# Optimization experiments

Hardware: AMD Instinct MI355X
Metric: run time of the kernel (lower is better)

Reference implementation:

```python
import jax, jax.numpy as jnp
import numpy as np

B, N, M, E, CD, H, DH, MH = 4, 2048, 512, 512, 256, 8, 64, 1024
EPS = 1e-6

def _ln(x):
    m = x.mean(-1, keepdims=True)
    v = ((x - m) ** 2).mean(-1, keepdims=True)
    return (x - m) / jnp.sqrt(v + EPS)

def _heads(t):  # [B, L, H*DH] -> [B, H, L, DH]
    b, l, _ = t.shape
    return t.reshape(b, l, H, DH).transpose(0, 2, 1, 3)

def _attn(q, k, v, scale):
    sim = jnp.einsum('bhid,bhjd->bhij', q, k) * scale
    a = jax.nn.softmax(sim, axis=-1)
    o = jnp.einsum('bhij,bhjd->bhid', a, v)
    b, h, l, d = o.shape
    return o.transpose(0, 2, 1, 3).reshape(b, l, h * d)

def setup_inputs() -> dict:
    key = jax.random.key(0)
    ks = jax.random.split(key, 16)
    s = 0.02
    return {
        'cond': jax.random.normal(ks[0], (B, M, CD), jnp.float32),
        'x_in': jax.random.normal(ks[1], (B, N, E), jnp.float32),
        # nn.MultiheadAttention params (combined in-proj + out-proj)
        'Wqkv': jax.random.normal(ks[2], (3 * E, E), jnp.float32) * s,
        'b_qkv': jnp.zeros((3 * E,), jnp.float32),
        'Wo': jax.random.normal(ks[3], (E, E), jnp.float32) * s,
        'bo': jnp.zeros((E,), jnp.float32),
        # CrossAttention params (q/k/v no bias, out has bias)
        'Wcq': jax.random.normal(ks[4], (H * DH, E), jnp.float32) * s,
        'Wck': jax.random.normal(ks[5], (H * DH, CD), jnp.float32) * s,
        'Wcv': jax.random.normal(ks[6], (H * DH, CD), jnp.float32) * s,
        'Wco': jax.random.normal(ks[7], (E, H * DH), jnp.float32) * s,
        'bco': jnp.zeros((E,), jnp.float32),
        # MLP params (note: ReLU applied after the LAST layer too, per source)
        'W1': jax.random.normal(ks[8], (MH, E), jnp.float32) * s,
        'b1': jnp.zeros((MH,), jnp.float32),
        'W2': jax.random.normal(ks[9], (E, MH), jnp.float32) * s,
        'b2': jnp.zeros((E,), jnp.float32),
    }

def reference(cond, x_in, Wqkv, b_qkv, Wo, bo, Wcq, Wck, Wcv, Wco, bco, W1, b1, W2, b2):
    # --- self-attention (nn.MultiheadAttention math) ---
    xn = _ln(x_in)
    qkv = xn @ Wqkv.T + b_qkv  # [B,N,3E]
    q, k, v = jnp.split(qkv, 3, axis=-1)
    sa = _attn(_heads(q), _heads(k), _heads(v), 1.0 / jnp.sqrt(jnp.float32(DH)))
    x = sa @ Wo.T + bo + x_in
    # --- cross-attention ---
    xn2 = _ln(x)
    cq = _heads(xn2 @ Wcq.T)
    ck = _heads(cond @ Wck.T)
    cv = _heads(cond @ Wcv.T)
    ca = _attn(cq, ck, cv, DH ** -0.5)
    x = ca @ Wco.T + bco + x
    # --- MLP (ReLU after both layers, as in source) ---
    xn3 = _ln(x)
    h = jax.nn.relu(xn3 @ W1.T + b1)
    m = jax.nn.relu(h @ W2.T + b2)
    return m + x
```

## Files before the change

kernel.cpp:

```cpp
#include <hip/hip_runtime.h>
#include <cstdint>
#include <cstddef>


typedef short short8 __attribute__((ext_vector_type(8)));
typedef short short4v __attribute__((ext_vector_type(4)));
typedef float f32x4 __attribute__((ext_vector_type(4)));
typedef float f32x16 __attribute__((ext_vector_type(16)));

typedef __attribute__((address_space(1))) const void gconst_t;
typedef __attribute__((address_space(3))) void lds_t;

__device__ __forceinline__ void gl_lds16(const void* g, void* l) {
  __builtin_amdgcn_global_load_lds((gconst_t*)g, (lds_t*)l, 16, 0, 0);
}

__device__ __forceinline__ short f2bf(float f) {
  union { float f; unsigned u; } x; x.f = f;
  unsigned r = x.u + 0x7fffu + ((x.u >> 16) & 1u);
  return (short)(r >> 16);
}

__device__ __forceinline__ void pl32swap(unsigned& a, unsigned& b) {
  asm("v_permlane32_swap_b32 %0, %1" : "+v"(a), "+v"(b));
}

struct CastDesc { const float* src; short* dst; int nblk; };
struct CastArgs { CastDesc d[9]; };

__global__ __launch_bounds__(256) void cast_multi(CastArgs a) {
  int bi = blockIdx.x;
#pragma unroll
  for (int i = 0; i < 9; ++i) {
    if (bi < a.d[i].nblk) {
      int idx = (bi * 256 + threadIdx.x) * 8;
      const float* src = a.d[i].src;
      float4 f0 = *(const float4*)(src + idx);
      float4 f1 = *(const float4*)(src + idx + 4);
      short8 o;
      o[0] = f2bf(f0.x); o[1] = f2bf(f0.y); o[2] = f2bf(f0.z); o[3] = f2bf(f0.w);
      o[4] = f2bf(f1.x); o[5] = f2bf(f1.y); o[6] = f2bf(f1.z); o[7] = f2bf(f1.w);
      *(short8*)(a.d[i].dst + idx) = o;
      return;
    }
    bi -= a.d[i].nblk;
  }
}

__global__ __launch_bounds__(256) void ln_kernel(
    const float* __restrict__ x, short* __restrict__ out, int nrows) {
  int row = blockIdx.x * 4 + (threadIdx.x >> 6);
  int lane = threadIdx.x & 63;
  if (row >= nrows) return;
  const float* xr = x + (size_t)row * 512 + lane * 8;
  float4 a = *(const float4*)xr;
  float4 b = *(const float4*)(xr + 4);
  float v[8] = {a.x, a.y, a.z, a.w, b.x, b.y, b.z, b.w};
  float s = 0.f;
#pragma unroll
  for (int e = 0; e < 8; ++e) s += v[e];
#pragma unroll
  for (int m = 1; m < 64; m <<= 1) s += __shfl_xor(s, m);
  float mean = s * (1.f / 512.f);
  float sq = 0.f;
#pragma unroll
  for (int e = 0; e < 8; ++e) { float d = v[e] - mean; sq += d * d; }
#pragma unroll
  for (int m = 1; m < 64; m <<= 1) sq += __shfl_xor(sq, m);
  float rstd = rsqrtf(sq * (1.f / 512.f) + 1e-6f);
  short8 o;
#pragma unroll
  for (int e = 0; e < 8; ++e) o[e] = f2bf((v[e] - mean) * rstd);
  *(short8*)(out + (size_t)row * 512 + lane * 8) = o;
}

template <int TN, bool BIAS, bool RELU, bool RES, bool OUTBF, bool VT>
__global__ __launch_bounds__(256) void gemm_nt(
    const short* __restrict__ A, const short* __restrict__ W,
    const float* __restrict__ bias, const float* __restrict__ res,
    void* __restrict__ outp, int R, int NC, int K, int gx,
    short* __restrict__ vt, int vcol0, int vn_log2,
    float oscale, int oscale_end) {
  constexpr int WN = TN / 2;
  constexpr int NF = WN / 16;
  __shared__ short As[3][128 * 32];
  __shared__ short Ws[3][TN * 32];
  const int nwg = gridDim.x;
  const int b0 = blockIdx.x;
  const int bid = ((nwg & 7) == 0) ? ((b0 & 7) * (nwg >> 3) + (b0 >> 3)) : b0;
  const int bx = bid % gx, by = bid / gx;
  const int brow = by * 128, bcol = bx * TN;
  const int t = threadIdx.x;
  const int wid = t >> 6, lane = t & 63;
  const int lr = lane & 15, lk = lane >> 4;
  const int wrow = (wid >> 1) * 64, wcol = (wid & 1) * WN;
  f32x4 acc[4][NF] = {};

  const int sra = wid * 32 + (lane >> 2);
  const int sca = (lane & 3) * 8;
  const short* Ag = A + (size_t)(brow + sra) * K + sca;
  const short* Wg;
  if constexpr (TN == 128) {
    Wg = W + (size_t)(bcol + sra) * K + sca;
  } else {
    Wg = W + (size_t)(bcol + wid * 16 + (lane >> 2)) * K + sca;
  }

#define G_STAGE(I, BUF)                                                       \
  {                                                                           \
    const int k0_ = (I) * 32;                                                 \
    gl_lds16(Ag + k0_, &As[BUF][wid * 1024]);                                 \
    gl_lds16(Ag + (size_t)16 * K + k0_, &As[BUF][wid * 1024 + 512]);          \
    if constexpr (TN == 128) {                                                \
      gl_lds16(Wg + k0_, &Ws[BUF][wid * 1024]);                               \
      gl_lds16(Wg + (size_t)16 * K + k0_, &Ws[BUF][wid * 1024 + 512]);        \
    } else {                                                                  \
      gl_lds16(Wg + k0_, &Ws[BUF][wid * 512]);                                \
    }                                                                         \
  }

  const int ns = K / 32;
  G_STAGE(0, 0);
  G_STAGE(1, 1);
  if constexpr (TN == 128)
    asm volatile("s_waitcnt vmcnt(4)" ::: "memory");
  else
    asm volatile("s_waitcnt vmcnt(3)" ::: "memory");
  __builtin_amdgcn_s_barrier();

  for (int i = 0; i < ns; ++i) {
    const int cur = i % 3;
    if (i + 2 < ns) G_STAGE(i + 2, (i + 2) % 3);

    short8 af[4], bf[NF];
#pragma unroll
    for (int mi = 0; mi < 4; ++mi)
      af[mi] = *(const short8*)&As[cur][(wrow + mi * 16 + lr) * 32 + lk * 8];
#pragma unroll
    for (int ni = 0; ni < NF; ++ni)
      bf[ni] = *(const short8*)&Ws[cur][(wcol + ni * 16 + lr) * 32 + lk * 8];
#pragma unroll
    for (int mi = 0; mi < 4; ++mi)
#pragma unroll
      for (int ni = 0; ni < NF; ++ni)
        acc[mi][ni] = __builtin_amdgcn_mfma_f32_16x16x32_bf16(
            af[mi], bf[ni], acc[mi][ni], 0, 0, 0);

    if (i + 1 < ns) {
      if (i + 2 < ns) {
        if constexpr (TN == 128)
          asm volatile("s_waitcnt vmcnt(4) lgkmcnt(0)" ::: "memory");
        else
          asm volatile("s_waitcnt vmcnt(3) lgkmcnt(0)" ::: "memory");
      } else {
        asm volatile("s_waitcnt vmcnt(0) lgkmcnt(0)" ::: "memory");
      }
      __builtin_amdgcn_s_barrier();
    }
  }
#undef G_STAGE

  if (VT && bcol >= vcol0) {
    const int vn_mask = (1 << vn_log2) - 1;
#pragma unroll
    for (int mi = 0; mi < 4; ++mi) {
#pragma unroll
      for (int ni = 0; ni < NF; ++ni) {
        int col = bcol + wcol + ni * 16 + lr;
        int vc = col - vcol0;
        int r0 = brow + wrow + mi * 16 + lk * 4;
        int bb = r0 >> vn_log2;
        int n = r0 & vn_mask;
        float bv = BIAS ? bias[col] : 0.f;
        short4v o;
#pragma unroll
        for (int j = 0; j < 4; ++j) o[j] = f2bf(acc[mi][ni][j] + bv);
        *(short4v*)(vt + (((size_t)(bb * 512 + vc)) << vn_log2) + n) = o;
      }
    }
    return;
  }

#pragma unroll
  for (int mi = 0; mi < 4; ++mi) {
#pragma unroll
    for (int ni = 0; ni < NF; ++ni) {
      int col = bcol + wcol + ni * 16 + lr;
      int row0 = brow + wrow + mi * 16 + lk * 4;
      float bv = BIAS ? bias[col] : 0.f;
#pragma unroll
      for (int j = 0; j < 4; ++j) {
        float v = acc[mi][ni][j] + bv;
        if (RELU) v = fmaxf(v, 0.f);
        if (col < oscale_end) v *= oscale;
        size_t oi = (size_t)(row0 + j) * NC + col;
        if (RES) v += res[oi];
        if (OUTBF) ((short*)outp)[oi] = f2bf(v);
        else       ((float*)outp)[oi] = v;
      }
    }
  }
}

__global__ __launch_bounds__(256) void flash_attn8(
    const short* __restrict__ q, const short* __restrict__ k,
    const short* __restrict__ vt, short* __restrict__ out,
    int qstride, int kstride, int Nq, int Nkv, int vn_log2, int H_) {
  __shared__ short Ks[2 * 128 * 64];
  __shared__ short Vs[2 * 64 * 128];
  const int t = threadIdx.x;
  const int wid = t >> 6, lane = t & 63;
  const int l31 = lane & 31, lh = lane >> 5;
  const int nb = gridDim.x;
  const int b0 = blockIdx.x;
  const int bid = ((nb & 7) == 0) ? ((b0 & 7) * (nb >> 3) + (b0 >> 3)) : b0;
  const int gx = Nq >> 7;
  const int bh = bid / gx, qblk = bid - bh * gx;
  const int b = bh / H_, h = bh - b * H_;
  const int q0 = qblk * 128 + wid * 32;

  short8 qf[4];
  {
    const short* qp = q + ((size_t)b * Nq + q0 + l31) * qstride + h * 64 + lh * 8;
#pragma unroll
    for (int kc = 0; kc < 4; ++kc) qf[kc] = *(const short8*)(qp + kc * 16);
  }

  f32x16 o0 = {}, o1 = {};
  f32x16 lacc = {};

  const int krw = lane >> 3;
  const short* kG = k + ((size_t)b * Nkv + wid * 32 + krw) * kstride + h * 64 +
                    (((lane & 7) ^ krw) << 3);
  const short* vGp[4];
#pragma unroll
  for (int j = 0; j < 4; ++j)
    vGp[j] = vt + (((size_t)bh * 64 + wid * 16 + j * 4 + (lane >> 4)) << vn_log2) +
             (((lane & 15) ^ (j * 4 + (lane >> 4))) << 3);
  short* kD = &Ks[wid * 2048];
  short* vD = &Vs[wid * 2048];

#define STAGE_KV(KT, BUF)                                                     \
  {                                                                           \
    const short* kp_ = kG + (size_t)(KT) * kstride;                           \
    short* kd_ = kD + (BUF) * 8192;                                           \
    gl_lds16(kp_, kd_);                                                       \
    gl_lds16(kp_ + (size_t)8 * kstride, kd_ + 512);                           \
    gl_lds16(kp_ + (size_t)16 * kstride, kd_ + 1024);                         \
    gl_lds16(kp_ + (size_t)24 * kstride, kd_ + 1536);                         \
    short* vd_ = vD + (BUF) * 8192;                                           \
    gl_lds16(vGp[0] + (KT), vd_);                                             \
    gl_lds16(vGp[1] + (KT), vd_ + 512);                                       \
    gl_lds16(vGp[2] + (KT), vd_ + 1024);                                      \
    gl_lds16(vGp[3] + (KT), vd_ + 1536);                                      \
  }

  STAGE_KV(0, 0);
  __syncthreads();
  int cur = 0;

  for (int kt = 0; kt < Nkv; kt += 128) {
    if (kt + 128 < Nkv) STAGE_KV(kt + 128, cur ^ 1);

    const short* kbase = &Ks[cur * 8192];
    const short* vbase = &Vs[cur * 8192];

#pragma unroll
    for (int kk = 0; kk < 4; ++kk) {
      f32x16 s = {};
      {
        const int r = kk * 32 + l31;
        const short* krow = kbase + r * 64;
        const int rx = r & 7;
#pragma unroll
        for (int kc = 0; kc < 4; ++kc) {
          short8 kf = *(const short8*)(krow + (((kc * 2 + lh) ^ rx) << 3));
          s = __builtin_amdgcn_mfma_f32_32x32x16_bf16(kf, qf[kc], s, 0, 0, 0);
        }
      }
#pragma unroll
      for (int rr = 0; rr < 16; ++rr)
        s[rr] = __builtin_amdgcn_exp2f(s[rr]);
      lacc += s;
      unsigned w[8];
#pragma unroll
      for (int g = 0; g < 8; ++g)
        asm("v_cvt_pk_bf16_f32 %0, %1, %2" : "=v"(w[g]) : "v"(s[2 * g]), "v"(s[2 * g + 1]));
      pl32swap(w[0], w[2]); pl32swap(w[1], w[3]);
      pl32swap(w[4], w[6]); pl32swap(w[5], w[7]);
      union { unsigned u[4]; short8 s8; } pf0, pf1;
      pf0.u[0] = w[0]; pf0.u[1] = w[1]; pf0.u[2] = w[2]; pf0.u[3] = w[3];
      pf1.u[0] = w[4]; pf1.u[1] = w[5]; pf1.u[2] = w[6]; pf1.u[3] = w[7];
#pragma unroll
      for (int ch = 0; ch < 2; ++ch) {
        short8 pf = ch ? pf1.s8 : pf0.s8;
        const int c16 = kk * 4 + ch * 2 + lh;
        {
          const int d = l31;
          short8 vf = *(const short8*)(vbase + d * 128 + ((c16 ^ (d & 15)) << 3));
          o0 = __builtin_amdgcn_mfma_f32_32x32x16_bf16(vf, pf, o0, 0, 0, 0);
        }
        {
          const int d = 32 + l31;
          short8 vf = *(const short8*)(vbase + d * 128 + ((c16 ^ (d & 15)) << 3));
          o1 = __builtin_amdgcn_mfma_f32_32x32x16_bf16(vf, pf, o1, 0, 0, 0);
        }
      }
    }

    __syncthreads();
    cur ^= 1;
  }
#undef STAGE_KV

  float ls = (((lacc[0] + lacc[1]) + (lacc[2] + lacc[3])) +
              ((lacc[4] + lacc[5]) + (lacc[6] + lacc[7]))) +
             (((lacc[8] + lacc[9]) + (lacc[10] + lacc[11])) +
              ((lacc[12] + lacc[13]) + (lacc[14] + lacc[15])));
  ls += __shfl_xor(ls, 32);
  float inv = 1.f / ls;

  short* orow = out + ((size_t)b * Nq + q0 + l31) * 512 + h * 64 + 4 * lh;
#pragma unroll
  for (int g = 0; g < 4; ++g) {
    short4v w0, w1;
#pragma unroll
    for (int j = 0; j < 4; ++j) {
      w0[j] = f2bf(o0[4 * g + j] * inv);
      w1[j] = f2bf(o1[4 * g + j] * inv);
    }
    *(short4v*)(orow + 8 * g) = w0;
    *(short4v*)(orow + 32 + 8 * g) = w1;
  }
}

extern "C" void kernel_launch(void* const* d_in, const int* in_sizes, int n_in,
                              void* d_out, int out_size, void* d_ws, size_t ws_size,
                              hipStream_t stream) {
  (void)in_sizes; (void)n_in; (void)out_size; (void)ws_size;
  const float* cond  = (const float*)d_in[0];
  const float* x_in  = (const float*)d_in[1];
  const float* Wqkv  = (const float*)d_in[2];
  const float* b_qkv = (const float*)d_in[3];
  const float* Wo    = (const float*)d_in[4];
  const float* bo    = (const float*)d_in[5];
  const float* Wcq   = (const float*)d_in[6];
  const float* Wck   = (const float*)d_in[7];
  const float* Wcv   = (const float*)d_in[8];
  const float* Wco   = (const float*)d_in[9];
  const float* bco   = (const float*)d_in[10];
  const float* W1    = (const float*)d_in[11];
  const float* b1    = (const float*)d_in[12];
  const float* W2    = (const float*)d_in[13];
  const float* b2    = (const float*)d_in[14];
  float* out = (float*)d_out;

  const int Bv = 4, Nv = 2048, Mv = 512, Ev = 512, Hv = 8, MHv = 1024, CDv = 256;
  const int RN = Bv * Nv;
  const int RM = Bv * Mv;
  const float KSC = 0.125f * 1.44269504f;

  char* ws = (char*)d_ws;
  size_t off = 0;
  auto alloc = [&](size_t bytes) { void* p = ws + off; off += bytes; return p; };

  short* wqkv_b = (short*)alloc((size_t)3 * Ev * Ev * 2);
  short* wo_b   = (short*)alloc((size_t)Ev * Ev * 2);
  short* wcq_b  = (short*)alloc((size_t)Ev * Ev * 2);
  short* wck_b  = (short*)alloc((size_t)Ev * CDv * 2);
  short* wcv_b  = (short*)alloc((size_t)Ev * CDv * 2);
  short* wco_b  = (short*)alloc((size_t)Ev * Ev * 2);
  short* w1_b   = (short*)alloc((size_t)MHv * Ev * 2);
  short* w2_b   = (short*)alloc((size_t)Ev * MHv * 2);
  short* cond_b = (short*)alloc((size_t)RM * CDv * 2);
  short* xnb    = (short*)alloc((size_t)RN * Ev * 2);
  short* sa_b   = (short*)alloc((size_t)RN * Ev * 2);
  float* x1     = (float*)alloc((size_t)RN * Ev * 4);
  float* x2     = (float*)alloc((size_t)RN * Ev * 4);
  char*  qreg   = (char*)alloc((size_t)RN * 3 * Ev * 2);
  short* qkv_b  = (short*)qreg;
  short* cq   = (short*)(qreg + 0);
  short* ck   = (short*)(qreg + (size_t)RN * Ev * 2);
  short* vt_c = (short*)(qreg + (size_t)RN * Ev * 2 + (size_t)4 * 1024 * 1024);
  short* ca   = (short*)(qreg + (size_t)RN * Ev * 2 + (size_t)6 * 1024 * 1024);
  short* hb   = (short*)(qreg + 0);
  short* vt_s = (short*)x2;

  CastArgs ca_args;
  const float* srcs[9] = {Wqkv, Wo, Wcq, Wck, Wcv, Wco, W1, W2, cond};
  short* dsts[9] = {wqkv_b, wo_b, wcq_b, wck_b, wcv_b, wco_b, w1_b, w2_b, cond_b};
  int ns[9] = {3*Ev*Ev, Ev*Ev, Ev*Ev, Ev*CDv, Ev*CDv, Ev*Ev, MHv*Ev, Ev*MHv, RM*CDv};
  int tot_blk = 0;
  for (int i = 0; i < 9; ++i) {
    ca_args.d[i].src = srcs[i]; ca_args.d[i].dst = dsts[i];
    ca_args.d[i].nblk = ns[i] / 2048; tot_blk += ca_args.d[i].nblk;
  }
  cast_multi<<<tot_blk, 256, 0, stream>>>(ca_args);

  dim3 blk(256);

  ln_kernel<<<RN / 4, blk, 0, stream>>>(x_in, xnb, RN);
  gemm_nt<128, true, false, false, true, true><<<(3 * Ev / 128) * (RN / 128), blk, 0, stream>>>(
      xnb, wqkv_b, b_qkv, nullptr, qkv_b, RN, 3 * Ev, Ev, 3 * Ev / 128,
      vt_s, 2 * Ev, 11, KSC, Ev);
  flash_attn8<<<(Nv / 128) * Bv * Hv, blk, 0, stream>>>(
      qkv_b, qkv_b + Ev, vt_s, sa_b, 3 * Ev, 3 * Ev, Nv, Nv, 11, Hv);
  gemm_nt<64, true, false, true, false, false><<<(Ev / 64) * (RN / 128), blk, 0, stream>>>(
      sa_b, wo_b, bo, x_in, x1, RN, Ev, Ev, Ev / 64, nullptr, 0, 0, 1.f, 0);
  ln_kernel<<<RN / 4, blk, 0, stream>>>(x1, xnb, RN);
  gemm_nt<64, false, false, false, true, false><<<(Ev / 64) * (RN / 128), blk, 0, stream>>>(
      xnb, wcq_b, nullptr, nullptr, cq, RN, Ev, Ev, Ev / 64, nullptr, 0, 0, KSC, Ev);
  gemm_nt<64, false, false, false, true, true><<<(2 * Ev / 64) * (RM / 128), blk, 0, stream>>>(
      cond_b, wck_b, nullptr, nullptr, ck, RM, 2 * Ev, CDv, 2 * Ev / 64,
      vt_c, Ev, 9, 1.f, 0);
  flash_attn8<<<(Nv / 128) * Bv * Hv, blk, 0, stream>>>(
      cq, ck, vt_c, ca, Ev, 2 * Ev, Nv, Mv, 9, Hv);
  gemm_nt<64, true, false, true, false, false><<<(Ev / 64) * (RN / 128), blk, 0, stream>>>(
      ca, wco_b, bco, x1, x2, RN, Ev, Ev, Ev / 64, nullptr, 0, 0, 1.f, 0);
  ln_kernel<<<RN / 4, blk, 0, stream>>>(x2, xnb, RN);
  gemm_nt<64, true, true, false, true, false><<<(MHv / 64) * (RN / 128), blk, 0, stream>>>(
      xnb, w1_b, b1, nullptr, hb, RN, MHv, Ev, MHv / 64, nullptr, 0, 0, 1.f, 0);
  gemm_nt<64, true, true, true, false, false><<<(Ev / 64) * (RN / 128), blk, 0, stream>>>(
      hb, w2_b, b2, x2, out, RN, Ev, MHv, Ev / 64, nullptr, 0, 0, 1.f, 0);
}
```

Measured before the change: 212.8 us.

## Use swizzled BK=64 GEMM tiles and store residual stream in bf16

The GEMM now uses a fixed 128x64 tile with a K step of 64 and XOR-swizzled LDS layout, which halves the barrier count per K and cuts LDS bank conflicts. The QKV GEMM drops its 128-wide tile in favour of this shape. The intermediate residual buffers x1 and x2 are stored as bf16 instead of fp32, and the LayerNorm and residual epilogues read bf16, which reduces memory traffic. The cost is lower precision in the residual stream and more, smaller QKV blocks.

```diff
diff --git a/kernel.cpp b/kernel.cpp
--- a/kernel.cpp
+++ b/kernel.cpp
@@ -19,6 +19,10 @@
   union { float f; unsigned u; } x; x.f = f;
   unsigned r = x.u + 0x7fffu + ((x.u >> 16) & 1u);
   return (short)(r >> 16);
+}
+__device__ __forceinline__ float bf2f(short s) {
+  union { unsigned u; float f; } x; x.u = ((unsigned)(unsigned short)s) << 16;
+  return x.f;
 }
 
 __device__ __forceinline__ void pl32swap(unsigned& a, unsigned& b) {
@@ -47,15 +51,25 @@
   }
 }
 
+template <bool INBF>
 __global__ __launch_bounds__(256) void ln_kernel(
-    const float* __restrict__ x, short* __restrict__ out, int nrows) {
+    const void* __restrict__ xin, short* __restrict__ out, int nrows) {
   int row = blockIdx.x * 4 + (threadIdx.x >> 6);
   int lane = threadIdx.x & 63;
   if (row >= nrows) return;
-  const float* xr = x + (size_t)row * 512 + lane * 8;
-  float4 a = *(const float4*)xr;
-  float4 b = *(const float4*)(xr + 4);
-  float v[8] = {a.x, a.y, a.z, a.w, b.x, b.y, b.z, b.w};
+  float v[8];
+  if constexpr (INBF) {
+    const short* xr = (const short*)xin + (size_t)row * 512 + lane * 8;
+    short8 a = *(const short8*)xr;
+#pragma unroll
+    for (int e = 0; e < 8; ++e) v[e] = bf2f(a[e]);
+  } else {
+    const float* xr = (const float*)xin + (size_t)row * 512 + lane * 8;
+    float4 a = *(const float4*)xr;
+    float4 b = *(const float4*)(xr + 4);
+    v[0] = a.x; v[1] = a.y; v[2] = a.z; v[3] = a.w;
+    v[4] = b.x; v[5] = b.y; v[6] = b.z; v[7] = b.w;
+  }
   float s = 0.f;
 #pragma unroll
   for (int e = 0; e < 8; ++e) s += v[e];
@@ -74,87 +88,78 @@
   *(short8*)(out + (size_t)row * 512 + lane * 8) = o;
 }
 
-template <int TN, bool BIAS, bool RELU, bool RES, bool OUTBF, bool VT>
+template <int RESMODE, bool BIAS, bool RELU, bool OUTBF, bool VT>
 __global__ __launch_bounds__(256) void gemm_nt(
     const short* __restrict__ A, const short* __restrict__ W,
-    const float* __restrict__ bias, const float* __restrict__ res,
+    const float* __restrict__ bias, const void* __restrict__ res,
     void* __restrict__ outp, int R, int NC, int K, int gx,
     short* __restrict__ vt, int vcol0, int vn_log2,
     float oscale, int oscale_end) {
-  constexpr int WN = TN / 2;
-  constexpr int NF = WN / 16;
-  __shared__ short As[3][128 * 32];
-  __shared__ short Ws[3][TN * 32];
+  __shared__ short As[3][128 * 64];
+  __shared__ short Ws[3][64 * 64];
   const int nwg = gridDim.x;
   const int b0 = blockIdx.x;
   const int bid = ((nwg & 7) == 0) ? ((b0 & 7) * (nwg >> 3) + (b0 >> 3)) : b0;
   const int bx = bid % gx, by = bid / gx;
-  const int brow = by * 128, bcol = bx * TN;
+  const int brow = by * 128, bcol = bx * 64;
   const int t = threadIdx.x;
   const int wid = t >> 6, lane = t & 63;
   const int lr = lane & 15, lk = lane >> 4;
-  const int wrow = (wid >> 1) * 64, wcol = (wid & 1) * WN;
-  f32x4 acc[4][NF] = {};
-
-  const int sra = wid * 32 + (lane >> 2);
-  const int sca = (lane & 3) * 8;
-  const short* Ag = A + (size_t)(brow + sra) * K + sca;
-  const short* Wg;
-  if constexpr (TN == 128) {
-    Wg = W + (size_t)(bcol + sra) * K + sca;
-  } else {
-    Wg = W + (size_t)(bcol + wid * 16 + (lane >> 2)) * K + sca;
-  }
+  const int wrow = (wid >> 1) * 64, wcol = (wid & 1) * 32;
+  f32x4 acc[4][2] = {};
+
+  const int srw = lane >> 3;
+  const int scol = (((lane & 7) ^ srw) << 3);
+  const short* Ag = A + (size_t)(brow + wid * 32 + srw) * K + scol;
+  const short* Wg = W + (size_t)(bcol + wid * 16 + srw) * K + scol;
 
 #define G_STAGE(I, BUF)                                                       \
   {                                                                           \
-    const int k0_ = (I) * 32;                                                 \
-    gl_lds16(Ag + k0_, &As[BUF][wid * 1024]);                                 \
-    gl_lds16(Ag + (size_t)16 * K + k0_, &As[BUF][wid * 1024 + 512]);          \
-    if constexpr (TN == 128) {                                                \
-      gl_lds16(Wg + k0_, &Ws[BUF][wid * 1024]);                               \
-      gl_lds16(Wg + (size_t)16 * K + k0_, &Ws[BUF][wid * 1024 + 512]);        \
-    } else {                                                                  \
-      gl_lds16(Wg + k0_, &Ws[BUF][wid * 512]);                                \
-    }                                                                         \
-  }
-
-  const int ns = K / 32;
+    const int k0_ = (I) * 64;                                                 \
+    gl_lds16(Ag + k0_, &As[BUF][(wid * 32) * 64]);                            \
+    gl_lds16(Ag + (size_t)8 * K + k0_, &As[BUF][(wid * 32 + 8) * 64]);        \
+    gl_lds16(Ag + (size_t)16 * K + k0_, &As[BUF][(wid * 32 + 16) * 64]);      \
+    gl_lds16(Ag + (size_t)24 * K + k0_, &As[BUF][(wid * 32 + 24) * 64]);      \
+    gl_lds16(Wg + k0_, &Ws[BUF][(wid * 16) * 64]);                            \
+    gl_lds16(Wg + (size_t)8 * K + k0_, &Ws[BUF][(wid * 16 + 8) * 64]);        \
+  }
+
+  const int ns = K / 64;
   G_STAGE(0, 0);
   G_STAGE(1, 1);
-  if constexpr (TN == 128)
-    asm volatile("s_waitcnt vmcnt(4)" ::: "memory");
-  else
-    asm volatile("s_waitcnt vmcnt(3)" ::: "memory");
+  asm volatile("s_waitcnt vmcnt(6)" ::: "memory");
   __builtin_amdgcn_s_barrier();
 
   for (int i = 0; i < ns; ++i) {
     const int cur = i % 3;
     if (i + 2 < ns) G_STAGE(i + 2, (i + 2) % 3);
 
-    short8 af[4], bf[NF];
-#pragma unroll
-    for (int mi = 0; mi < 4; ++mi)
-      af[mi] = *(const short8*)&As[cur][(wrow + mi * 16 + lr) * 32 + lk * 8];
-#pragma unroll
-    for (int ni = 0; ni < NF; ++ni)
-      bf[ni] = *(const short8*)&Ws[cur][(wcol + ni * 16 + lr) * 32 + lk * 8];
-#pragma unroll
-    for (int mi = 0; mi < 4; ++mi)
-#pragma unroll
-      for (int ni = 0; ni < NF; ++ni)
-        acc[mi][ni] = __builtin_amdgcn_mfma_f32_16x16x32_bf16(
-            af[mi], bf[ni], acc[mi][ni], 0, 0, 0);
+#pragma unroll
+    for (int kc = 0; kc < 2; ++kc) {
+      short8 af[4], bf[2];
+#pragma unroll
+      for (int mi = 0; mi < 4; ++mi) {
+        const int row = wrow + mi * 16 + lr;
+        af[mi] = *(const short8*)&As[cur][row * 64 + (((kc * 4 + lk) ^ (row & 7)) << 3)];
+      }
+#pragma unroll
+      for (int ni = 0; ni < 2; ++ni) {
+        const int row = wcol + ni * 16 + lr;
+        bf[ni] = *(const short8*)&Ws[cur][row * 64 + (((kc * 4 + lk) ^ (row & 7)) << 3)];
+      }
+#pragma unroll
+      for (int mi = 0; mi < 4; ++mi)
+#pragma unroll
+        for (int ni = 0; ni < 2; ++ni)
+          acc[mi][ni] = __builtin_amdgcn_mfma_f32_16x16x32_bf16(
+              af[mi], bf[ni], acc[mi][ni], 0, 0, 0);
+    }
 
     if (i + 1 < ns) {
-      if (i + 2 < ns) {
-        if constexpr (TN == 128)
-          asm volatile("s_waitcnt vmcnt(4) lgkmcnt(0)" ::: "memory");
-        else
-          asm volatile("s_waitcnt vmcnt(3) lgkmcnt(0)" ::: "memory");
-      } else {
+      if (i + 2 < ns)
+        asm volatile("s_waitcnt vmcnt(6) lgkmcnt(0)" ::: "memory");
+      else
         asm volatile("s_waitcnt vmcnt(0) lgkmcnt(0)" ::: "memory");
-      }
       __builtin_amdgcn_s_barrier();
     }
   }
@@ -165,7 +170,7 @@
 #pragma unroll
     for (int mi = 0; mi < 4; ++mi) {
 #pragma unroll
-      for (int ni = 0; ni < NF; ++ni) {
+      for (int ni = 0; ni < 2; ++ni) {
         int col = bcol + wcol + ni * 16 + lr;
         int vc = col - vcol0;
         int r0 = brow + wrow + mi * 16 + lk * 4;
@@ -184,7 +189,7 @@
 #pragma unroll
   for (int mi = 0; mi < 4; ++mi) {
 #pragma unroll
-    for (int ni = 0; ni < NF; ++ni) {
+    for (int ni = 0; ni < 2; ++ni) {
       int col = bcol + wcol + ni * 16 + lr;
       int row0 = brow + wrow + mi * 16 + lk * 4;
       float bv = BIAS ? bias[col] : 0.f;
@@ -194,7 +199,8 @@
         if (RELU) v = fmaxf(v, 0.f);
         if (col < oscale_end) v *= oscale;
         size_t oi = (size_t)(row0 + j) * NC + col;
-        if (RES) v += res[oi];
+        if (RESMODE == 1) v += ((const float*)res)[oi];
+        if (RESMODE == 2) v += bf2f(((const short*)res)[oi]);
         if (OUTBF) ((short*)outp)[oi] = f2bf(v);
         else       ((float*)outp)[oi] = v;
       }
@@ -375,8 +381,8 @@
   short* cond_b = (short*)alloc((size_t)RM * CDv * 2);
   short* xnb    = (short*)alloc((size_t)RN * Ev * 2);
   short* sa_b   = (short*)alloc((size_t)RN * Ev * 2);
-  float* x1     = (float*)alloc((size_t)RN * Ev * 4);
-  float* x2     = (float*)alloc((size_t)RN * Ev * 4);
+  short* x1     = (short*)alloc((size_t)RN * Ev * 2);
+  short* x2     = (short*)alloc((size_t)RN * Ev * 2);
   char*  qreg   = (char*)alloc((size_t)RN * 3 * Ev * 2);
   short* qkv_b  = (short*)qreg;
   short* cq   = (short*)(qreg + 0);
@@ -389,37 +395,37 @@
   CastArgs ca_args;
   const float* srcs[9] = {Wqkv, Wo, Wcq, Wck, Wcv, Wco, W1, W2, cond};
   short* dsts[9] = {wqkv_b, wo_b, wcq_b, wck_b, wcv_b, wco_b, w1_b, w2_b, cond_b};
-  int ns[9] = {3*Ev*Ev, Ev*Ev, Ev*Ev, Ev*CDv, Ev*CDv, Ev*Ev, MHv*Ev, Ev*MHv, RM*CDv};
+  int ns_[9] = {3*Ev*Ev, Ev*Ev, Ev*Ev, Ev*CDv, Ev*CDv, Ev*Ev, MHv*Ev, Ev*MHv, RM*CDv};
   int tot_blk = 0;
   for (int i = 0; i < 9; ++i) {
     ca_args.d[i].src = srcs[i]; ca_args.d[i].dst = dsts[i];
-    ca_args.d[i].nblk = ns[i] / 2048; tot_blk += ca_args.d[i].nblk;
+    ca_args.d[i].nblk = ns_[i] / 2048; tot_blk += ca_args.d[i].nblk;
   }
   cast_multi<<<tot_blk, 256, 0, stream>>>(ca_args);
 
   dim3 blk(256);
 
-  ln_kernel<<<RN / 4, blk, 0, stream>>>(x_in, xnb, RN);
-  gemm_nt<128, true, false, false, true, true><<<(3 * Ev / 128) * (RN / 128), blk, 0, stream>>>(
-      xnb, wqkv_b, b_qkv, nullptr, qkv_b, RN, 3 * Ev, Ev, 3 * Ev / 128,
+  ln_kernel<false><<<RN / 4, blk, 0, stream>>>(x_in, xnb, RN);
+  gemm_nt<0, true, false, true, true><<<(3 * Ev / 64) * (RN / 128), blk, 0, stream>>>(
+      xnb, wqkv_b, b_qkv, nullptr, qkv_b, RN, 3 * Ev, Ev, 3 * Ev / 64,
       vt_s, 2 * Ev, 11, KSC, Ev);
   flash_attn8<<<(Nv / 128) * Bv * Hv, blk, 0, stream>>>(
       qkv_b, qkv_b + Ev, vt_s, sa_b, 3 * Ev, 3 * Ev, Nv, Nv, 11, Hv);
-  gemm_nt<64, true, false, true, false, false><<<(Ev / 64) * (RN / 128), blk, 0, stream>>>(
+  gemm_nt<1, true, false, true, false><<<(Ev / 64) * (RN / 128), blk, 0, stream>>>(
       sa_b, wo_b, bo, x_in, x1, RN, Ev, Ev, Ev / 64, nullptr, 0, 0, 1.f, 0);
-  ln_kernel<<<RN / 4, blk, 0, stream>>>(x1, xnb, RN);
-  gemm_nt<64, false, false, false, true, false><<<(Ev / 64) * (RN / 128), blk, 0, stream>>>(
+  ln_kernel<true><<<RN / 4, blk, 0, stream>>>(x1, xnb, RN);
+  gemm_nt<0, false, false, true, false><<<(Ev / 64) * (RN / 128), blk, 0, stream>>>(
       xnb, wcq_b, nullptr, nullptr, cq, RN, Ev, Ev, Ev / 64, nullptr, 0, 0, KSC, Ev);
-  gemm_nt<64, false, false, false, true, true><<<(2 * Ev / 64) * (RM / 128), blk, 0, stream>>>(
+  gemm_nt<0, false, false, true, true><<<(2 * Ev / 64) * (RM / 128), blk, 0, stream>>>(
       cond_b, wck_b, nullptr, nullptr, ck, RM, 2 * Ev, CDv, 2 * Ev / 64,
       vt_c, Ev, 9, 1.f, 0);
   flash_attn8<<<(Nv / 128) * Bv * Hv, blk, 0, stream>>>(
       cq, ck, vt_c, ca, Ev, 2 * Ev, Nv, Mv, 9, Hv);
-  gemm_nt<64, true, false, true, false, false><<<(Ev / 64) * (RN / 128), blk, 0, stream>>>(
+  gemm_nt<2, true, false, true, false><<<(Ev / 64) * (RN / 128), blk, 0, stream>>>(
       ca, wco_b, bco, x1, x2, RN, Ev, Ev, Ev / 64, nullptr, 0, 0, 1.f, 0);
-  ln_kernel<<<RN / 4, blk, 0, stream>>>(x2, xnb, RN);
-  gemm_nt<64, true, true, false, true, false><<<(MHv / 64) * (RN / 128), blk, 0, stream>>>(
+  ln_kernel<true><<<RN / 4, blk, 0, stream>>>(x2, xnb, RN);
+  gemm_nt<0, true, true, true, false><<<(MHv / 64) * (RN / 128), blk, 0, stream>>>(
       xnb, w1_b, b1, nullptr, hb, RN, MHv, Ev, MHv / 64, nullptr, 0, 0, 1.f, 0);
-  gemm_nt<64, true, true, true, false, false><<<(Ev / 64) * (RN / 128), blk, 0, stream>>>(
+  gemm_nt<2, true, true, false, false><<<(Ev / 64) * (RN / 128), blk, 0, stream>>>(
       hb, w2_b, b2, x2, out, RN, Ev, MHv, Ev / 64, nullptr, 0, 0, 1.f, 0);
 }
```

Result: faster. 195.8 us (-8.0%).
